# Performance work log

Hardware: AMD Instinct MI355X
Metric: run time of the kernel (lower is better)

Reference implementation:

```python
import jax, jax.numpy as jnp
import numpy as np

HEADS = 8
DIM_HEAD = 128
ATTN_MATRIX_SCALE = 1.5  # tau applied to mean-centered logits
SCALE = DIM_HEAD ** -0.5


def setup_inputs() -> dict:
    key = jax.random.key(0)
    ks = jax.random.split(key, 7)
    b, n, m = 2, 2048, 2048
    qd, cd, inner = 1024, 768, HEADS * DIM_HEAD
    x = jax.random.normal(ks[0], (b, n, qd), dtype=jnp.float32)
    context = jax.random.normal(ks[1], (b, m, cd), dtype=jnp.float32)
    Wq = jax.random.normal(ks[2], (qd, inner), dtype=jnp.float32) * (qd ** -0.5)
    Wk = jax.random.normal(ks[3], (cd, inner), dtype=jnp.float32) * (cd ** -0.5)
    Wv = jax.random.normal(ks[4], (cd, inner), dtype=jnp.float32) * (cd ** -0.5)
    Wout = jax.random.normal(ks[5], (inner, qd), dtype=jnp.float32) * (inner ** -0.5)
    bout = jnp.zeros((qd,), dtype=jnp.float32)
    return {"x": x, "context": context, "Wq": Wq, "Wk": Wk, "Wv": Wv,
            "Wout": Wout, "bout": bout}


def _split_heads(t):
    # (b, n, h*d) -> (h, b*n, d); matches rearrange '(b h) n d -> h (b n) d'
    b, n, _ = t.shape
    t = t.reshape(b, n, HEADS, DIM_HEAD)
    return t.transpose(2, 0, 1, 3).reshape(HEADS, b * n, DIM_HEAD)


def reference(x, context, Wq, Wk, Wv, Wout, bout):
    b, n, _ = x.shape
    qh = _split_heads(jnp.einsum('bnq,qi->bni', x, Wq))        # (h, b*n, d)
    kh = _split_heads(jnp.einsum('bmc,ci->bmi', context, Wk))  # (h, b*m, d)
    vh = _split_heads(jnp.einsum('bmc,ci->bmi', context, Wv))  # (h, b*m, d)

    # custom mean-centered / tau-scaled similarity (_compute_sim_with_tau)
    sim = jnp.einsum('hid,hjd->hij', qh, kh) * SCALE
    mean = jnp.mean(sim, axis=-1, keepdims=True)
    sim = (sim - mean) * ATTN_MATRIX_SCALE + mean

    attn = jax.nn.softmax(sim, axis=-1)
    out = jnp.einsum('hij,hjd->hid', attn, vh)                 # (h, b*n, d)

    # (h, b*n, d) -> (b, n, h*d)
    out = out.reshape(HEADS, b, n, DIM_HEAD).transpose(1, 2, 0, 3)
    out = out.reshape(b, n, HEADS * DIM_HEAD)
    return jnp.einsum('bni,iq->bnq', out, Wout) + bout
```

## Files before the change

### kernel.cpp

```cpp
#include <hip/hip_runtime.h>
#include <cstdint>
#include <cstddef>

typedef unsigned short u16t;
typedef __bf16 bf16x8_t __attribute__((ext_vector_type(8)));
typedef float f32x4_t __attribute__((ext_vector_type(4)));
typedef float f32x16_t __attribute__((ext_vector_type(16)));

#define MFMA_BF16 __builtin_amdgcn_mfma_f32_16x16x32_bf16
#define MFMA32    __builtin_amdgcn_mfma_f32_32x32x16_bf16

__device__ __forceinline__ u16t f2bf(float f) {
    uint32_t u = __builtin_bit_cast(uint32_t, f);
    u += 0x7fffu + ((u >> 16) & 1u);
    return (u16t)(u >> 16);
}

__device__ __forceinline__ uint32_t pk2bf(float a, float b) {
    return (uint32_t)f2bf(a) | ((uint32_t)f2bf(b) << 16);
}

__device__ __forceinline__ float bflo(uint32_t u) {
    return __builtin_bit_cast(float, u << 16);
}
__device__ __forceinline__ float bfhi(uint32_t u) {
    return __builtin_bit_cast(float, u & 0xffff0000u);
}

__device__ __forceinline__ bf16x8_t ld_frag(const u16t* p) {
    return __builtin_bit_cast(bf16x8_t, *(const uint4*)p);
}

__device__ __forceinline__ uint32_t cvtpk(float lo, float hi) {
    uint32_t r;
    asm("v_cvt_pk_bf16_f32 %0, %1, %2" : "=v"(r) : "v"(lo), "v"(hi));
    return r;
}
__device__ __forceinline__ void swap32(uint32_t& a, uint32_t& b) {
    asm("v_permlane32_swap_b32 %0, %1" : "+v"(a), "+v"(b));
}

__device__ __forceinline__ void gl_lds16(const u16t* g, u16t* l) {
    __builtin_amdgcn_global_load_lds(
        (const __attribute__((address_space(1))) void*)g,
        (__attribute__((address_space(3))) void*)l, 16, 0, 0);
}

__global__ void cast2_bf16_kernel(const float* __restrict__ s0, u16t* __restrict__ d0, int n0,
                                  const float* __restrict__ s1, u16t* __restrict__ d1, int n1) {
    int i = blockIdx.x * blockDim.x + threadIdx.x;
    const float* s; u16t* d;
    if (i < n0) { s = s0; d = d0; }
    else { i -= n0; if (i >= n1) return; s = s1; d = d1; }
    float4 v = ((const float4*)s)[i];
    uint2 o;
    o.x = pk2bf(v.x, v.y);
    o.y = pk2bf(v.z, v.w);
    ((uint2*)d)[i] = o;
}

__global__ void transpose4_kernel(const float* __restrict__ Wq, const float* __restrict__ Wk,
                                  const float* __restrict__ Wv, const float* __restrict__ Wo,
                                  u16t* __restrict__ Wqt, u16t* __restrict__ Wkt,
                                  u16t* __restrict__ Wvt, u16t* __restrict__ Wot) {
    const int z = blockIdx.z;
    const float* W = z == 0 ? Wq : (z == 1 ? Wk : (z == 2 ? Wv : Wo));
    u16t* Wt      = z == 0 ? Wqt : (z == 1 ? Wkt : (z == 2 ? Wvt : Wot));
    const int K   = (z == 1 || z == 2) ? 768 : 1024;
    const int N = 1024;
    int n0 = blockIdx.x * 32, k0 = blockIdx.y * 32;
    if (k0 >= K) return;
    __shared__ float tile[32][33];
    int tx = threadIdx.x, ty = threadIdx.y;
    for (int i = ty; i < 32; i += 8)
        tile[i][tx] = W[(size_t)(k0 + i) * N + n0 + tx];
    __syncthreads();
    for (int i = ty; i < 32; i += 8)
        Wt[(size_t)(n0 + i) * K + k0 + tx] = f2bf(tile[tx][i]);
}

__device__ __forceinline__ void gemm_core(
    const u16t* __restrict__ A, const u16t* __restrict__ Bt,
    int K, void* __restrict__ outp, const float* __restrict__ bias,
    int mode, float oscale, int bm, int bn)
{
    __shared__ __align__(16) u16t As[2][128 * 64];
    __shared__ __align__(16) u16t Bs[2][64 * 64];
    const int tid = threadIdx.x;
    const int wave = tid >> 6, lane = tid & 63;
    const int wm = wave & 1, wn = wave >> 1;
    const int quad = lane >> 4, l16 = lane & 15;

    const int l8r = lane >> 3, l8c = lane & 7;
    const int cgx = (l8c ^ l8r) * 8;

    f32x4_t acc[4][2];
#pragma unroll
    for (int i = 0; i < 4; ++i)
#pragma unroll
        for (int j = 0; j < 2; ++j) acc[i][j] = (f32x4_t){0.f, 0.f, 0.f, 0.f};

    const int nk = K >> 6;

#pragma unroll
    for (int it = 0; it < 4; ++it) {
        int rb = wave * 32 + it * 8;
        gl_lds16(&A[(size_t)(bm + rb + l8r) * K + cgx], &As[0][rb * 64]);
    }
#pragma unroll
    for (int it = 0; it < 2; ++it) {
        int rb = wave * 16 + it * 8;
        gl_lds16(&Bt[(size_t)(bn + rb + l8r) * K + cgx], &Bs[0][rb * 64]);
    }

    for (int ki = 0; ki < nk; ++ki) {
        const int buf = ki & 1;
        __syncthreads();

        if (ki + 1 < nk) {
            const int kc = (ki + 1) << 6;
#pragma unroll
            for (int it = 0; it < 4; ++it) {
                int rb = wave * 32 + it * 8;
                gl_lds16(&A[(size_t)(bm + rb + l8r) * K + kc + cgx], &As[buf ^ 1][rb * 64]);
            }
#pragma unroll
            for (int it = 0; it < 2; ++it) {
                int rb = wave * 16 + it * 8;
                gl_lds16(&Bt[(size_t)(bn + rb + l8r) * K + kc + cgx], &Bs[buf ^ 1][rb * 64]);
            }
        }

#pragma unroll
        for (int ks = 0; ks < 2; ++ks) {
            bf16x8_t af[4], bfv[2];
#pragma unroll
            for (int i = 0; i < 4; ++i) {
                int r = wm * 64 + i * 16 + l16;
                af[i] = ld_frag(&As[buf][r * 64 + (((ks * 4 + quad) ^ (r & 7)) * 8)]);
            }
#pragma unroll
            for (int j = 0; j < 2; ++j) {
                int r = wn * 32 + j * 16 + l16;
                bfv[j] = ld_frag(&Bs[buf][r * 64 + (((ks * 4 + quad) ^ (r & 7)) * 8)]);
            }
#pragma unroll
            for (int i = 0; i < 4; ++i)
#pragma unroll
                for (int j = 0; j < 2; ++j)
                    acc[i][j] = MFMA_BF16(af[i], bfv[j], acc[i][j], 0, 0, 0);
        }
    }

    if (mode == 3) {
        float* out = (float*)outp;
#pragma unroll
        for (int j = 0; j < 2; ++j) {
            int c = bn + wn * 32 + j * 16 + l16;
            float b = bias[c];
#pragma unroll
            for (int i = 0; i < 4; ++i) {
                int rb = bm + wm * 64 + i * 16 + quad * 4;
#pragma unroll
                for (int r = 0; r < 4; ++r)
                    out[(size_t)(rb + r) * 1024 + c] = acc[i][j][r] + b;
            }
        }
    } else if (mode == 2) {
        u16t* out = (u16t*)outp;
#pragma unroll
        for (int i = 0; i < 4; ++i)
#pragma unroll
            for (int j = 0; j < 2; ++j) {
                int rb = bm + wm * 64 + i * 16 + quad * 4;
                int c = bn + wn * 32 + j * 16 + l16;
                int h = c >> 7, d = c & 127;
                uint2 pk;
                pk.x = pk2bf(acc[i][j][0], acc[i][j][1]);
                pk.y = pk2bf(acc[i][j][2], acc[i][j][3]);
                *(uint2*)&out[((size_t)h * 128 + d) * 4096 + rb] = pk;
            }
    } else {
        u16t* out = (u16t*)outp;
#pragma unroll
        for (int i = 0; i < 4; ++i)
#pragma unroll
            for (int j = 0; j < 2; ++j) {
                int rb = bm + wm * 64 + i * 16 + quad * 4;
                int c = bn + wn * 32 + j * 16 + l16;
                int h = c >> 7, d = c & 127;
#pragma unroll
                for (int r = 0; r < 4; ++r)
                    out[((size_t)h * 4096 + rb + r) * 128 + d] = f2bf(acc[i][j][r] * oscale);
            }
    }
}

__global__ __launch_bounds__(256) void gemm_bf16_kernel(
    const u16t* __restrict__ A, const u16t* __restrict__ Bt,
    int K, void* __restrict__ outp, const float* __restrict__ bias,
    int mode, float oscale)
{
    gemm_core(A, Bt, K, outp, bias, mode, oscale, blockIdx.y * 128, blockIdx.x * 64);
}

__global__ __launch_bounds__(256) void qkv_kernel(
    const u16t* __restrict__ x_bf, const u16t* __restrict__ ctx_bf,
    const u16t* __restrict__ Wqt, const u16t* __restrict__ Wkt,
    const u16t* __restrict__ Wvt,
    u16t* __restrict__ Qh, u16t* __restrict__ Kh, u16t* __restrict__ Vt,
    float qscale)
{
    const int z = blockIdx.z;
    const u16t* A  = (z == 0) ? x_bf : ctx_bf;
    const u16t* Bt = (z == 0) ? Wqt : ((z == 1) ? Wkt : Wvt);
    void* outp     = (z == 0) ? (void*)Qh : ((z == 1) ? (void*)Kh : (void*)Vt);
    const int K    = (z == 0) ? 1024 : 768;
    const int mode = (z == 2) ? 2 : 0;
    const float sc = (z == 0) ? qscale : 1.0f;
    gemm_core(A, Bt, K, outp, nullptr, mode, sc, blockIdx.y * 128, blockIdx.x * 64);
}

__global__ __launch_bounds__(256) void flash_kernel(
    const u16t* __restrict__ Qh, const u16t* __restrict__ Kh,
    const u16t* __restrict__ Vtg, u16t* __restrict__ Op0,
    u16t* __restrict__ Op1, float* __restrict__ lp)
{
    extern __shared__ __align__(16) u16t smem[];
    const int h = blockIdx.y;
    const int q0 = blockIdx.x * 128;
    const int z = blockIdx.z;
    const int tid = threadIdx.x;
    const int wave = tid >> 6, lane = tid & 63;
    const int l31 = lane & 31, hh = lane >> 5;

    const u16t* Kg = Kh + (size_t)h * 4096 * 128 + (size_t)z * 2048 * 128;
    const u16t* Vg = Vtg + (size_t)h * 128 * 4096 + z * 2048;

    {
        const u16t* Qg = Qh + ((size_t)h * 4096 + q0) * 128;
#pragma unroll
        for (int it = 0; it < 8; ++it) {
            int slot = it * 256 + tid;
            int r = slot >> 4, c = slot & 15;
            uint4 v = *(const uint4*)&Qg[(size_t)r * 128 + c * 8];
            *(uint4*)&smem[r * 128 + ((c ^ (r & 15)) * 8)] = v;
        }
    }
    __syncthreads();
    bf16x8_t qf[8];
    {
        int r = wave * 32 + l31;
#pragma unroll
        for (int s = 0; s < 8; ++s)
            qf[s] = ld_frag(&smem[r * 128 + (((s * 2 + hh) ^ (r & 15)) * 8)]);
    }
    __syncthreads();

    const bool kRole = wave < 2;
    const int wh = wave & 1;
    const int rK = lane >> 4, cK = lane & 15;
    const int rV = lane >> 2, cV = lane & 3;

    if (kRole) {
#pragma unroll
        for (int it = 0; it < 4; ++it) {
            int is = wh * 4 + it;
            int rowL = is * 4 + rK;
            gl_lds16(Kg + (size_t)rowL * 128 + ((cK ^ (rowL & 15)) * 8),
                     smem + is * 512);
        }
    } else {
#pragma unroll
        for (int it = 0; it < 4; ++it) {
            int is = wh * 4 + it;
            int rowL = is * 16 + rV;
            gl_lds16(Vg + (size_t)rowL * 4096 + ((cV ^ (rowL & 3)) * 8),
                     smem + 8192 + is * 512);
        }
    }

    f32x16_t O[4];
#pragma unroll
    for (int dg = 0; dg < 4; ++dg)
#pragma unroll
        for (int r = 0; r < 16; ++r) O[dg][r] = 0.f;
    float lsum = 0.f;

    for (int kb = 0; kb < 64; ++kb) {
        const int buf = kb & 1;
        __syncthreads();

        if (kb < 63) {
            const int j0 = (kb + 1) * 32;
            const int bo = (buf ^ 1) * 4096;
            if (kRole) {
#pragma unroll
                for (int it = 0; it < 4; ++it) {
                    int is = wh * 4 + it;
                    int rowL = is * 4 + rK;
                    gl_lds16(Kg + (size_t)(j0 + rowL) * 128 + ((cK ^ (rowL & 15)) * 8),
                             smem + bo + is * 512);
                }
            } else {
#pragma unroll
                for (int it = 0; it < 4; ++it) {
                    int is = wh * 4 + it;
                    int rowL = is * 16 + rV;
                    gl_lds16(Vg + (size_t)rowL * 4096 + j0 + ((cV ^ (rowL & 3)) * 8),
                             smem + 8192 + bo + is * 512);
                }
            }
        }

        const u16t* Ks = smem + buf * 4096;
        const u16t* Vs = smem + 8192 + buf * 4096;

        f32x16_t Sa, Sb;
#pragma unroll
        for (int r = 0; r < 16; ++r) { Sa[r] = 0.f; Sb[r] = 0.f; }
        const int swz = l31 & 15;
#pragma unroll
        for (int s = 0; s < 8; s += 2) {
            bf16x8_t k0 = ld_frag(&Ks[l31 * 128 + (((s * 2 + hh) ^ swz) * 8)]);
            bf16x8_t k1 = ld_frag(&Ks[l31 * 128 + ((((s + 1) * 2 + hh) ^ swz) * 8)]);
            Sa = MFMA32(k0, qf[s], Sa, 0, 0, 0);
            Sb = MFMA32(k1, qf[s + 1], Sb, 0, 0, 0);
        }

        float p[16];
#pragma unroll
        for (int r = 0; r < 16; ++r)
            p[r] = __builtin_amdgcn_exp2f(Sa[r] + Sb[r]);
        lsum += ((((p[0] + p[1]) + (p[2] + p[3])) + ((p[4] + p[5]) + (p[6] + p[7])))
              + (((p[8] + p[9]) + (p[10] + p[11])) + ((p[12] + p[13]) + (p[14] + p[15]))));

        uint32_t w0 = cvtpk(p[0], p[1]),   w2 = cvtpk(p[4], p[5]);
        uint32_t w1 = cvtpk(p[2], p[3]),   w3 = cvtpk(p[6], p[7]);
        swap32(w0, w2); swap32(w1, w3);
        uint32_t y0 = cvtpk(p[8], p[9]),   y2 = cvtpk(p[12], p[13]);
        uint32_t y1 = cvtpk(p[10], p[11]), y3 = cvtpk(p[14], p[15]);
        swap32(y0, y2); swap32(y1, y3);
        uint4 pw0; pw0.x = w0; pw0.y = w1; pw0.z = w2; pw0.w = w3;
        uint4 pw1; pw1.x = y0; pw1.y = y1; pw1.z = y2; pw1.w = y3;
        bf16x8_t pf0 = __builtin_bit_cast(bf16x8_t, pw0);
        bf16x8_t pf1 = __builtin_bit_cast(bf16x8_t, pw1);

#pragma unroll
        for (int dg = 0; dg < 4; ++dg) {
            int rv = dg * 32 + l31;
            int vsw = rv & 3;
            bf16x8_t v0 = ld_frag(&Vs[rv * 32 + ((hh ^ vsw) * 8)]);
            bf16x8_t v1 = ld_frag(&Vs[rv * 32 + (((2 + hh) ^ vsw) * 8)]);
            O[dg] = MFMA32(v0, pf0, O[dg], 0, 0, 0);
            O[dg] = MFMA32(v1, pf1, O[dg], 0, 0, 0);
        }
    }

    lsum += __shfl_xor(lsum, 32, 64);
    u16t* Op = z ? Op1 : Op0;
    const int qrow = q0 + wave * 32 + l31;
    if (lane < 32) lp[z * 32768 + qrow * 8 + h] = lsum;
#pragma unroll
    for (int dg = 0; dg < 4; ++dg)
#pragma unroll
        for (int rq = 0; rq < 4; ++rq) {
            uint2 pk;
            pk.x = pk2bf(O[dg][rq * 4 + 0], O[dg][rq * 4 + 1]);
            pk.y = pk2bf(O[dg][rq * 4 + 2], O[dg][rq * 4 + 3]);
            *(uint2*)&Op[(size_t)qrow * 1024 + h * 128 + dg * 32 + rq * 8 + hh * 4] = pk;
        }
}

__global__ __launch_bounds__(256) void combine_kernel(
    const u16t* __restrict__ O0, const u16t* __restrict__ O1,
    const float* __restrict__ lp, u16t* __restrict__ out)
{
    int t = blockIdx.x * blockDim.x + threadIdx.x;
    int e = t << 3;
    int i = e >> 10, h = (e >> 7) & 7;
    float inv = 1.f / (lp[i * 8 + h] + lp[32768 + i * 8 + h]);
    uint4 a = ((const uint4*)O0)[t];
    uint4 b = ((const uint4*)O1)[t];
    uint4 r;
    r.x = pk2bf((bflo(a.x) + bflo(b.x)) * inv, (bfhi(a.x) + bfhi(b.x)) * inv);
    r.y = pk2bf((bflo(a.y) + bflo(b.y)) * inv, (bfhi(a.y) + bfhi(b.y)) * inv);
    r.z = pk2bf((bflo(a.z) + bflo(b.z)) * inv, (bfhi(a.z) + bfhi(b.z)) * inv);
    r.w = pk2bf((bflo(a.w) + bflo(b.w)) * inv, (bfhi(a.w) + bfhi(b.w)) * inv);
    ((uint4*)out)[t] = r;
}

extern "C" void kernel_launch(void* const* d_in, const int* in_sizes, int n_in,
                              void* d_out, int out_size, void* d_ws, size_t ws_size,
                              hipStream_t stream)
{
    (void)in_sizes; (void)n_in; (void)out_size; (void)ws_size;
    const float* x    = (const float*)d_in[0];
    const float* ctx  = (const float*)d_in[1];
    const float* Wq   = (const float*)d_in[2];
    const float* Wk   = (const float*)d_in[3];
    const float* Wv   = (const float*)d_in[4];
    const float* Wout = (const float*)d_in[5];
    const float* bout = (const float*)d_in[6];
    float* out = (float*)d_out;

    u16t* ws = (u16t*)d_ws;
    u16t* x_bf   = ws;
    u16t* ctx_bf = x_bf + 4194304;
    u16t* Wqt    = ctx_bf + 3145728;
    u16t* Wkt    = Wqt + 1048576;
    u16t* Wvt    = Wkt + 786432;
    u16t* Woutt  = Wvt + 786432;
    u16t* Qh     = Woutt + 1048576;
    u16t* Kh     = Qh + 4194304;
    u16t* Vt     = Kh + 4194304;
    u16t* Oh   = x_bf;
    u16t* Ohp1 = ws + 4194304;
    float* lp  = (float*)(ws + 8388608);

    constexpr float QSCALE = 1.5f * 0.08838834764831845f * 1.4426950408889634f;

    (void)hipFuncSetAttribute((const void*)flash_kernel,
                              hipFuncAttributeMaxDynamicSharedMemorySize, 32768);

    cast2_bf16_kernel<<<7168, 256, 0, stream>>>(x, x_bf, 1048576, ctx, ctx_bf, 786432);
    transpose4_kernel<<<dim3(32, 32, 4), dim3(32, 8), 0, stream>>>(
        Wq, Wk, Wv, Wout, Wqt, Wkt, Wvt, Woutt);

    qkv_kernel<<<dim3(16, 32, 3), 256, 0, stream>>>(
        x_bf, ctx_bf, Wqt, Wkt, Wvt, Qh, Kh, Vt, QSCALE);

    flash_kernel<<<dim3(32, 8, 2), 256, 32768, stream>>>(Qh, Kh, Vt, Oh, Ohp1, lp);
    combine_kernel<<<2048, 256, 0, stream>>>(Oh, Ohp1, lp, Oh);

    gemm_bf16_kernel<<<dim3(16, 32), 256, 0, stream>>>(Oh, Woutt, 1024, out, bout, 3, 1.0f);
}
```

Before: 254.2 us.

## Process two 32-row query groups per wave in flash attention to reuse K/V fragments

Each wave of the flash kernel now owns 64 query rows, in two 32-row groups, instead of 32. Every K and V fragment loaded from LDS feeds twice as many MFMAs, and the number of blocks that stream K/V through shared memory is halved. The grid shrinks to 256 blocks with 64KB of dynamic shared memory for Q staging, and launch bounds allow one block per CU. The cost is a large rise in register use for the doubled accumulators and Q fragments, and only four waves per CU to hide latency.

```diff
diff --git a/kernel.cpp b/kernel.cpp
--- a/kernel.cpp
+++ b/kernel.cpp
@@ -221,14 +221,14 @@
     gemm_core(A, Bt, K, outp, nullptr, mode, sc, blockIdx.y * 128, blockIdx.x * 64);
 }
 
-__global__ __launch_bounds__(256) void flash_kernel(
+__global__ __launch_bounds__(256, 1) void flash_kernel(
     const u16t* __restrict__ Qh, const u16t* __restrict__ Kh,
     const u16t* __restrict__ Vtg, u16t* __restrict__ Op0,
     u16t* __restrict__ Op1, float* __restrict__ lp)
 {
     extern __shared__ __align__(16) u16t smem[];
     const int h = blockIdx.y;
-    const int q0 = blockIdx.x * 128;
+    const int q0 = blockIdx.x * 256;
     const int z = blockIdx.z;
     const int tid = threadIdx.x;
     const int wave = tid >> 6, lane = tid & 63;
@@ -240,7 +240,7 @@
     {
         const u16t* Qg = Qh + ((size_t)h * 4096 + q0) * 128;
 #pragma unroll
-        for (int it = 0; it < 8; ++it) {
+        for (int it = 0; it < 16; ++it) {
             int slot = it * 256 + tid;
             int r = slot >> 4, c = slot & 15;
             uint4 v = *(const uint4*)&Qg[(size_t)r * 128 + c * 8];
@@ -248,12 +248,13 @@
         }
     }
     __syncthreads();
-    bf16x8_t qf[8];
-    {
-        int r = wave * 32 + l31;
+    bf16x8_t qf[2][8];
+#pragma unroll
+    for (int g = 0; g < 2; ++g) {
+        int r = wave * 64 + g * 32 + l31;
 #pragma unroll
         for (int s = 0; s < 8; ++s)
-            qf[s] = ld_frag(&smem[r * 128 + (((s * 2 + hh) ^ (r & 15)) * 8)]);
+            qf[g][s] = ld_frag(&smem[r * 128 + (((s * 2 + hh) ^ (r & 15)) * 8)]);
     }
     __syncthreads();
 
@@ -280,12 +281,15 @@
         }
     }
 
-    f32x16_t O[4];
-#pragma unroll
-    for (int dg = 0; dg < 4; ++dg)
-#pragma unroll
-        for (int r = 0; r < 16; ++r) O[dg][r] = 0.f;
-    float lsum = 0.f;
+    f32x16_t O[2][4];
+#pragma unroll
+    for (int g = 0; g < 2; ++g)
+#pragma unroll
+        for (int dg = 0; dg < 4; ++dg)
+#pragma unroll
+            for (int r = 0; r < 16; ++r) O[g][dg][r] = 0.f;
+    float lsum0 = 0.f, lsum1 = 0.f;
+    const int swz = l31 & 15;
 
     for (int kb = 0; kb < 64; ++kb) {
         const int buf = kb & 1;
@@ -316,35 +320,56 @@
         const u16t* Ks = smem + buf * 4096;
         const u16t* Vs = smem + 8192 + buf * 4096;
 
-        f32x16_t Sa, Sb;
-#pragma unroll
-        for (int r = 0; r < 16; ++r) { Sa[r] = 0.f; Sb[r] = 0.f; }
-        const int swz = l31 & 15;
+        f32x16_t S0a, S0b, S1a, S1b;
+#pragma unroll
+        for (int r = 0; r < 16; ++r) { S0a[r] = 0.f; S0b[r] = 0.f; S1a[r] = 0.f; S1b[r] = 0.f; }
 #pragma unroll
         for (int s = 0; s < 8; s += 2) {
             bf16x8_t k0 = ld_frag(&Ks[l31 * 128 + (((s * 2 + hh) ^ swz) * 8)]);
             bf16x8_t k1 = ld_frag(&Ks[l31 * 128 + ((((s + 1) * 2 + hh) ^ swz) * 8)]);
-            Sa = MFMA32(k0, qf[s], Sa, 0, 0, 0);
-            Sb = MFMA32(k1, qf[s + 1], Sb, 0, 0, 0);
-        }
-
-        float p[16];
-#pragma unroll
-        for (int r = 0; r < 16; ++r)
-            p[r] = __builtin_amdgcn_exp2f(Sa[r] + Sb[r]);
-        lsum += ((((p[0] + p[1]) + (p[2] + p[3])) + ((p[4] + p[5]) + (p[6] + p[7])))
-              + (((p[8] + p[9]) + (p[10] + p[11])) + ((p[12] + p[13]) + (p[14] + p[15]))));
-
-        uint32_t w0 = cvtpk(p[0], p[1]),   w2 = cvtpk(p[4], p[5]);
-        uint32_t w1 = cvtpk(p[2], p[3]),   w3 = cvtpk(p[6], p[7]);
-        swap32(w0, w2); swap32(w1, w3);
-        uint32_t y0 = cvtpk(p[8], p[9]),   y2 = cvtpk(p[12], p[13]);
-        uint32_t y1 = cvtpk(p[10], p[11]), y3 = cvtpk(p[14], p[15]);
-        swap32(y0, y2); swap32(y1, y3);
-        uint4 pw0; pw0.x = w0; pw0.y = w1; pw0.z = w2; pw0.w = w3;
-        uint4 pw1; pw1.x = y0; pw1.y = y1; pw1.z = y2; pw1.w = y3;
-        bf16x8_t pf0 = __builtin_bit_cast(bf16x8_t, pw0);
-        bf16x8_t pf1 = __builtin_bit_cast(bf16x8_t, pw1);
+            S0a = MFMA32(k0, qf[0][s], S0a, 0, 0, 0);
+            S1a = MFMA32(k0, qf[1][s], S1a, 0, 0, 0);
+            S0b = MFMA32(k1, qf[0][s + 1], S0b, 0, 0, 0);
+            S1b = MFMA32(k1, qf[1][s + 1], S1b, 0, 0, 0);
+        }
+
+        bf16x8_t pf[2][2];
+        {
+            float p[16];
+#pragma unroll
+            for (int r = 0; r < 16; ++r)
+                p[r] = __builtin_amdgcn_exp2f(S0a[r] + S0b[r]);
+            lsum0 += ((((p[0] + p[1]) + (p[2] + p[3])) + ((p[4] + p[5]) + (p[6] + p[7])))
+                   + (((p[8] + p[9]) + (p[10] + p[11])) + ((p[12] + p[13]) + (p[14] + p[15]))));
+            uint32_t w0 = cvtpk(p[0], p[1]),   w2 = cvtpk(p[4], p[5]);
+            uint32_t w1 = cvtpk(p[2], p[3]),   w3 = cvtpk(p[6], p[7]);
+            swap32(w0, w2); swap32(w1, w3);
+            uint32_t y0 = cvtpk(p[8], p[9]),   y2 = cvtpk(p[12], p[13]);
+            uint32_t y1 = cvtpk(p[10], p[11]), y3 = cvtpk(p[14], p[15]);
+            swap32(y0, y2); swap32(y1, y3);
+            uint4 pw0; pw0.x = w0; pw0.y = w1; pw0.z = w2; pw0.w = w3;
+            uint4 pw1; pw1.x = y0; pw1.y = y1; pw1.z = y2; pw1.w = y3;
+            pf[0][0] = __builtin_bit_cast(bf16x8_t, pw0);
+            pf[0][1] = __builtin_bit_cast(bf16x8_t, pw1);
+        }
+        {
+            float p[16];
+#pragma unroll
+            for (int r = 0; r < 16; ++r)
+                p[r] = __builtin_amdgcn_exp2f(S1a[r] + S1b[r]);
+            lsum1 += ((((p[0] + p[1]) + (p[2] + p[3])) + ((p[4] + p[5]) + (p[6] + p[7])))
+                   + (((p[8] + p[9]) + (p[10] + p[11])) + ((p[12] + p[13]) + (p[14] + p[15]))));
+            uint32_t w0 = cvtpk(p[0], p[1]),   w2 = cvtpk(p[4], p[5]);
+            uint32_t w1 = cvtpk(p[2], p[3]),   w3 = cvtpk(p[6], p[7]);
+            swap32(w0, w2); swap32(w1, w3);
+            uint32_t y0 = cvtpk(p[8], p[9]),   y2 = cvtpk(p[12], p[13]);
+            uint32_t y1 = cvtpk(p[10], p[11]), y3 = cvtpk(p[14], p[15]);
+            swap32(y0, y2); swap32(y1, y3);
+            uint4 pw0; pw0.x = w0; pw0.y = w1; pw0.z = w2; pw0.w = w3;
+            uint4 pw1; pw1.x = y0; pw1.y = y1; pw1.z = y2; pw1.w = y3;
+            pf[1][0] = __builtin_bit_cast(bf16x8_t, pw0);
+            pf[1][1] = __builtin_bit_cast(bf16x8_t, pw1);
+        }
 
 #pragma unroll
         for (int dg = 0; dg < 4; ++dg) {
@@ -352,24 +377,30 @@
             int vsw = rv & 3;
             bf16x8_t v0 = ld_frag(&Vs[rv * 32 + ((hh ^ vsw) * 8)]);
             bf16x8_t v1 = ld_frag(&Vs[rv * 32 + (((2 + hh) ^ vsw) * 8)]);
-            O[dg] = MFMA32(v0, pf0, O[dg], 0, 0, 0);
-            O[dg] = MFMA32(v1, pf1, O[dg], 0, 0, 0);
-        }
-    }
-
-    lsum += __shfl_xor(lsum, 32, 64);
+            O[0][dg] = MFMA32(v0, pf[0][0], O[0][dg], 0, 0, 0);
+            O[0][dg] = MFMA32(v1, pf[0][1], O[0][dg], 0, 0, 0);
+            O[1][dg] = MFMA32(v0, pf[1][0], O[1][dg], 0, 0, 0);
+            O[1][dg] = MFMA32(v1, pf[1][1], O[1][dg], 0, 0, 0);
+        }
+    }
+
     u16t* Op = z ? Op1 : Op0;
-    const int qrow = q0 + wave * 32 + l31;
-    if (lane < 32) lp[z * 32768 + qrow * 8 + h] = lsum;
-#pragma unroll
-    for (int dg = 0; dg < 4; ++dg)
-#pragma unroll
-        for (int rq = 0; rq < 4; ++rq) {
-            uint2 pk;
-            pk.x = pk2bf(O[dg][rq * 4 + 0], O[dg][rq * 4 + 1]);
-            pk.y = pk2bf(O[dg][rq * 4 + 2], O[dg][rq * 4 + 3]);
-            *(uint2*)&Op[(size_t)qrow * 1024 + h * 128 + dg * 32 + rq * 8 + hh * 4] = pk;
-        }
+#pragma unroll
+    for (int g = 0; g < 2; ++g) {
+        float ls = g ? lsum1 : lsum0;
+        ls += __shfl_xor(ls, 32, 64);
+        const int qrow = q0 + wave * 64 + g * 32 + l31;
+        if (lane < 32) lp[z * 32768 + qrow * 8 + h] = ls;
+#pragma unroll
+        for (int dg = 0; dg < 4; ++dg)
+#pragma unroll
+            for (int rq = 0; rq < 4; ++rq) {
+                uint2 pk;
+                pk.x = pk2bf(O[g][dg][rq * 4 + 0], O[g][dg][rq * 4 + 1]);
+                pk.y = pk2bf(O[g][dg][rq * 4 + 2], O[g][dg][rq * 4 + 3]);
+                *(uint2*)&Op[(size_t)qrow * 1024 + h * 128 + dg * 32 + rq * 8 + hh * 4] = pk;
+            }
+    }
 }
 
 __global__ __launch_bounds__(256) void combine_kernel(
@@ -421,7 +452,7 @@
     constexpr float QSCALE = 1.5f * 0.08838834764831845f * 1.4426950408889634f;
 
     (void)hipFuncSetAttribute((const void*)flash_kernel,
-                              hipFuncAttributeMaxDynamicSharedMemorySize, 32768);
+                              hipFuncAttributeMaxDynamicSharedMemorySize, 65536);
 
     cast2_bf16_kernel<<<7168, 256, 0, stream>>>(x, x_bf, 1048576, ctx, ctx_bf, 786432);
     transpose4_kernel<<<dim3(32, 32, 4), dim3(32, 8), 0, stream>>>(
@@ -430,7 +461,7 @@
     qkv_kernel<<<dim3(16, 32, 3), 256, 0, stream>>>(
         x_bf, ctx_bf, Wqt, Wkt, Wvt, Qh, Kh, Vt, QSCALE);
 
-    flash_kernel<<<dim3(32, 8, 2), 256, 32768, stream>>>(Qh, Kh, Vt, Oh, Ohp1, lp);
+    flash_kernel<<<dim3(16, 8, 2), 256, 65536, stream>>>(Qh, Kh, Vt, Oh, Ohp1, lp);
     combine_kernel<<<2048, 256, 0, stream>>>(Oh, Ohp1, lp, Oh);
 
     gemm_bf16_kernel<<<dim3(16, 32), 256, 0, stream>>>(Oh, Woutt, 1024, out, bout, 3, 1.0f);
```

After: 255.3 us. About the same (+0.5%).

## Warp-specialize flash kernel into QK/softmax and PV producer-consumer waves

Applied to the files above, without the earlier changes.

Splits the flash attention block into two wave roles. Two waves compute QK^T and the exponentials for 64 query rows each and write bf16 P tiles to a double-buffered LDS region. The other two waves consume those tiles one step later, multiplying by V for a 64-column slice of the head dimension. The aim is to overlap the softmax/exp work with the PV MFMAs and stop recomputing fragments per wave. It costs an extra LDS round trip for P and more shared memory (53 KB), and adds launch bounds targeting 2 blocks per CU; each role also has idle MFMA phases.

```diff
diff --git a/kernel.cpp b/kernel.cpp
--- a/kernel.cpp
+++ b/kernel.cpp
@@ -221,7 +221,7 @@
     gemm_core(A, Bt, K, outp, nullptr, mode, sc, blockIdx.y * 128, blockIdx.x * 64);
 }
 
-__global__ __launch_bounds__(256) void flash_kernel(
+__global__ __launch_bounds__(256, 2) void flash_kernel(
     const u16t* __restrict__ Qh, const u16t* __restrict__ Kh,
     const u16t* __restrict__ Vtg, u16t* __restrict__ Op0,
     u16t* __restrict__ Op1, float* __restrict__ lp)
@@ -233,39 +233,28 @@
     const int tid = threadIdx.x;
     const int wave = tid >> 6, lane = tid & 63;
     const int l31 = lane & 31, hh = lane >> 5;
+    const int NT = 64;
 
     const u16t* Kg = Kh + (size_t)h * 4096 * 128 + (size_t)z * 2048 * 128;
     const u16t* Vg = Vtg + (size_t)h * 128 * 4096 + z * 2048;
 
-    {
-        const u16t* Qg = Qh + ((size_t)h * 4096 + q0) * 128;
-#pragma unroll
-        for (int it = 0; it < 8; ++it) {
-            int slot = it * 256 + tid;
-            int r = slot >> 4, c = slot & 15;
-            uint4 v = *(const uint4*)&Qg[(size_t)r * 128 + c * 8];
-            *(uint4*)&smem[r * 128 + ((c ^ (r & 15)) * 8)] = v;
-        }
-    }
-    __syncthreads();
-    bf16x8_t qf[8];
-    {
-        int r = wave * 32 + l31;
-#pragma unroll
-        for (int s = 0; s < 8; ++s)
-            qf[s] = ld_frag(&smem[r * 128 + (((s * 2 + hh) ^ (r & 15)) * 8)]);
-    }
-    __syncthreads();
-
-    const bool kRole = wave < 2;
-    const int wh = wave & 1;
+    const bool sRole = wave < 2;
     const int rK = lane >> 4, cK = lane & 15;
     const int rV = lane >> 2, cV = lane & 3;
 
-    if (kRole) {
+    bf16x8_t qf[2][8];
+    if (sRole) {
+        const u16t* Qg = Qh + ((size_t)h * 4096 + q0) * 128;
+#pragma unroll
+        for (int c = 0; c < 2; ++c) {
+            int qr = wave * 64 + c * 32 + l31;
+#pragma unroll
+            for (int s = 0; s < 8; ++s)
+                qf[c][s] = ld_frag(&Qg[(size_t)qr * 128 + s * 16 + hh * 8]);
+        }
 #pragma unroll
         for (int it = 0; it < 4; ++it) {
-            int is = wh * 4 + it;
+            int is = wave * 4 + it;
             int rowL = is * 4 + rK;
             gl_lds16(Kg + (size_t)rowL * 128 + ((cK ^ (rowL & 15)) * 8),
                      smem + is * 512);
@@ -273,103 +262,137 @@
     } else {
 #pragma unroll
         for (int it = 0; it < 4; ++it) {
-            int is = wh * 4 + it;
+            int is = (wave - 2) * 4 + it;
             int rowL = is * 16 + rV;
             gl_lds16(Vg + (size_t)rowL * 4096 + ((cV ^ (rowL & 3)) * 8),
                      smem + 8192 + is * 512);
         }
     }
 
-    f32x16_t O[4];
-#pragma unroll
-    for (int dg = 0; dg < 4; ++dg)
-#pragma unroll
-        for (int r = 0; r < 16; ++r) O[dg][r] = 0.f;
-    float lsum = 0.f;
-
-    for (int kb = 0; kb < 64; ++kb) {
-        const int buf = kb & 1;
+    f32x16_t O[2][4];
+#pragma unroll
+    for (int dg = 0; dg < 2; ++dg)
+#pragma unroll
+        for (int qc = 0; qc < 4; ++qc)
+#pragma unroll
+            for (int r = 0; r < 16; ++r) O[dg][qc][r] = 0.f;
+    float lsum[2] = {0.f, 0.f};
+
+    for (int t = 0; t <= NT; ++t) {
         __syncthreads();
 
-        if (kb < 63) {
-            const int j0 = (kb + 1) * 32;
-            const int bo = (buf ^ 1) * 4096;
-            if (kRole) {
-#pragma unroll
-                for (int it = 0; it < 4; ++it) {
-                    int is = wh * 4 + it;
-                    int rowL = is * 4 + rK;
-                    gl_lds16(Kg + (size_t)(j0 + rowL) * 128 + ((cK ^ (rowL & 15)) * 8),
-                             smem + bo + is * 512);
-                }
-            } else {
-#pragma unroll
-                for (int it = 0; it < 4; ++it) {
-                    int is = wh * 4 + it;
-                    int rowL = is * 16 + rV;
-                    gl_lds16(Vg + (size_t)rowL * 4096 + j0 + ((cV ^ (rowL & 3)) * 8),
-                             smem + 8192 + bo + is * 512);
-                }
-            }
-        }
-
-        const u16t* Ks = smem + buf * 4096;
-        const u16t* Vs = smem + 8192 + buf * 4096;
-
-        f32x16_t Sa, Sb;
-#pragma unroll
-        for (int r = 0; r < 16; ++r) { Sa[r] = 0.f; Sb[r] = 0.f; }
-        const int swz = l31 & 15;
-#pragma unroll
-        for (int s = 0; s < 8; s += 2) {
-            bf16x8_t k0 = ld_frag(&Ks[l31 * 128 + (((s * 2 + hh) ^ swz) * 8)]);
-            bf16x8_t k1 = ld_frag(&Ks[l31 * 128 + ((((s + 1) * 2 + hh) ^ swz) * 8)]);
-            Sa = MFMA32(k0, qf[s], Sa, 0, 0, 0);
-            Sb = MFMA32(k1, qf[s + 1], Sb, 0, 0, 0);
-        }
-
-        float p[16];
-#pragma unroll
-        for (int r = 0; r < 16; ++r)
-            p[r] = __builtin_amdgcn_exp2f(Sa[r] + Sb[r]);
-        lsum += ((((p[0] + p[1]) + (p[2] + p[3])) + ((p[4] + p[5]) + (p[6] + p[7])))
-              + (((p[8] + p[9]) + (p[10] + p[11])) + ((p[12] + p[13]) + (p[14] + p[15]))));
-
-        uint32_t w0 = cvtpk(p[0], p[1]),   w2 = cvtpk(p[4], p[5]);
-        uint32_t w1 = cvtpk(p[2], p[3]),   w3 = cvtpk(p[6], p[7]);
-        swap32(w0, w2); swap32(w1, w3);
-        uint32_t y0 = cvtpk(p[8], p[9]),   y2 = cvtpk(p[12], p[13]);
-        uint32_t y1 = cvtpk(p[10], p[11]), y3 = cvtpk(p[14], p[15]);
-        swap32(y0, y2); swap32(y1, y3);
-        uint4 pw0; pw0.x = w0; pw0.y = w1; pw0.z = w2; pw0.w = w3;
-        uint4 pw1; pw1.x = y0; pw1.y = y1; pw1.z = y2; pw1.w = y3;
-        bf16x8_t pf0 = __builtin_bit_cast(bf16x8_t, pw0);
-        bf16x8_t pf1 = __builtin_bit_cast(bf16x8_t, pw1);
-
-#pragma unroll
-        for (int dg = 0; dg < 4; ++dg) {
-            int rv = dg * 32 + l31;
-            int vsw = rv & 3;
-            bf16x8_t v0 = ld_frag(&Vs[rv * 32 + ((hh ^ vsw) * 8)]);
-            bf16x8_t v1 = ld_frag(&Vs[rv * 32 + (((2 + hh) ^ vsw) * 8)]);
-            O[dg] = MFMA32(v0, pf0, O[dg], 0, 0, 0);
-            O[dg] = MFMA32(v1, pf1, O[dg], 0, 0, 0);
-        }
-    }
-
-    lsum += __shfl_xor(lsum, 32, 64);
+        if (sRole) {
+            if (t < NT) {
+                if (t + 1 < NT) {
+                    const int j0 = (t + 1) * 32;
+                    u16t* kd = smem + ((t + 1) & 1) * 4096;
+#pragma unroll
+                    for (int it = 0; it < 4; ++it) {
+                        int is = wave * 4 + it;
+                        int rowL = is * 4 + rK;
+                        gl_lds16(Kg + (size_t)(j0 + rowL) * 128 + ((cK ^ (rowL & 15)) * 8),
+                                 kd + is * 512);
+                    }
+                }
+                const u16t* kb = smem + (t & 1) * 4096;
+                u16t* pw = smem + 16384 + (t & 1) * 5120;
+
+                f32x16_t S0, S1;
+#pragma unroll
+                for (int r = 0; r < 16; ++r) { S0[r] = 0.f; S1[r] = 0.f; }
+#pragma unroll
+                for (int s = 0; s < 8; ++s) {
+                    bf16x8_t kf = ld_frag(&kb[l31 * 128 + (((s * 2 + hh) ^ (l31 & 15)) * 8)]);
+                    S0 = MFMA32(kf, qf[0][s], S0, 0, 0, 0);
+                    S1 = MFMA32(kf, qf[1][s], S1, 0, 0, 0);
+                }
+
+#pragma unroll
+                for (int c = 0; c < 2; ++c) {
+                    float p[16];
+#pragma unroll
+                    for (int r = 0; r < 16; ++r)
+                        p[r] = __builtin_amdgcn_exp2f(c ? S1[r] : S0[r]);
+                    lsum[c] += ((((p[0] + p[1]) + (p[2] + p[3])) + ((p[4] + p[5]) + (p[6] + p[7])))
+                             + (((p[8] + p[9]) + (p[10] + p[11])) + ((p[12] + p[13]) + (p[14] + p[15]))));
+                    uint32_t w0 = cvtpk(p[0], p[1]),   w2 = cvtpk(p[4], p[5]);
+                    uint32_t w1 = cvtpk(p[2], p[3]),   w3 = cvtpk(p[6], p[7]);
+                    swap32(w0, w2); swap32(w1, w3);
+                    uint32_t y0 = cvtpk(p[8], p[9]),   y2 = cvtpk(p[12], p[13]);
+                    uint32_t y1 = cvtpk(p[10], p[11]), y3 = cvtpk(p[14], p[15]);
+                    swap32(y0, y2); swap32(y1, y3);
+                    uint4 pw0; pw0.x = w0; pw0.y = w1; pw0.z = w2; pw0.w = w3;
+                    uint4 pw1; pw1.x = y0; pw1.y = y1; pw1.z = y2; pw1.w = y3;
+                    int qloc = wave * 64 + c * 32 + l31;
+                    *(uint4*)&pw[qloc * 40 + hh * 8] = pw0;
+                    *(uint4*)&pw[qloc * 40 + 16 + hh * 8] = pw1;
+                }
+            }
+        } else {
+            if (t >= 1) {
+                if (t < NT) {
+                    const int j0 = t * 32;
+                    u16t* vd = smem + 8192 + (t & 1) * 4096;
+#pragma unroll
+                    for (int it = 0; it < 4; ++it) {
+                        int is = (wave - 2) * 4 + it;
+                        int rowL = is * 16 + rV;
+                        gl_lds16(Vg + (size_t)rowL * 4096 + j0 + ((cV ^ (rowL & 3)) * 8),
+                                 vd + is * 512);
+                    }
+                }
+                const u16t* vb = smem + 8192 + ((t - 1) & 1) * 4096;
+                const u16t* pb = smem + 16384 + ((t - 1) & 1) * 5120;
+
+                bf16x8_t pf[4][2];
+#pragma unroll
+                for (int qc = 0; qc < 4; ++qc)
+#pragma unroll
+                    for (int ks = 0; ks < 2; ++ks)
+                        pf[qc][ks] = ld_frag(&pb[(qc * 32 + l31) * 40 + ks * 16 + hh * 8]);
+#pragma unroll
+                for (int dg = 0; dg < 2; ++dg) {
+                    int rv = (wave - 2) * 64 + dg * 32 + l31;
+                    int vsw = rv & 3;
+                    bf16x8_t v0 = ld_frag(&vb[rv * 32 + ((hh ^ vsw) * 8)]);
+                    bf16x8_t v1 = ld_frag(&vb[rv * 32 + (((2 + hh) ^ vsw) * 8)]);
+#pragma unroll
+                    for (int qc = 0; qc < 4; ++qc) {
+                        O[dg][qc] = MFMA32(v0, pf[qc][0], O[dg][qc], 0, 0, 0);
+                        O[dg][qc] = MFMA32(v1, pf[qc][1], O[dg][qc], 0, 0, 0);
+                    }
+                }
+            }
+        }
+    }
+
     u16t* Op = z ? Op1 : Op0;
-    const int qrow = q0 + wave * 32 + l31;
-    if (lane < 32) lp[z * 32768 + qrow * 8 + h] = lsum;
-#pragma unroll
-    for (int dg = 0; dg < 4; ++dg)
-#pragma unroll
-        for (int rq = 0; rq < 4; ++rq) {
-            uint2 pk;
-            pk.x = pk2bf(O[dg][rq * 4 + 0], O[dg][rq * 4 + 1]);
-            pk.y = pk2bf(O[dg][rq * 4 + 2], O[dg][rq * 4 + 3]);
-            *(uint2*)&Op[(size_t)qrow * 1024 + h * 128 + dg * 32 + rq * 8 + hh * 4] = pk;
-        }
+    if (sRole) {
+#pragma unroll
+        for (int c = 0; c < 2; ++c) {
+            float ls = lsum[c];
+            ls += __shfl_xor(ls, 32, 64);
+            if (hh == 0) {
+                int qrow = q0 + wave * 64 + c * 32 + l31;
+                lp[z * 32768 + qrow * 8 + h] = ls;
+            }
+        }
+    } else {
+        const int wvoff = (wave - 2) * 64;
+#pragma unroll
+        for (int qc = 0; qc < 4; ++qc) {
+            size_t base = (size_t)(q0 + qc * 32 + l31) * 1024 + h * 128;
+#pragma unroll
+            for (int dg = 0; dg < 2; ++dg)
+#pragma unroll
+                for (int g = 0; g < 4; ++g) {
+                    uint2 pk;
+                    pk.x = pk2bf(O[dg][qc][g * 4 + 0], O[dg][qc][g * 4 + 1]);
+                    pk.y = pk2bf(O[dg][qc][g * 4 + 2], O[dg][qc][g * 4 + 3]);
+                    *(uint2*)&Op[base + wvoff + dg * 32 + g * 8 + hh * 4] = pk;
+                }
+        }
+    }
 }
 
 __global__ __launch_bounds__(256) void combine_kernel(
@@ -421,7 +444,7 @@
     constexpr float QSCALE = 1.5f * 0.08838834764831845f * 1.4426950408889634f;
 
     (void)hipFuncSetAttribute((const void*)flash_kernel,
-                              hipFuncAttributeMaxDynamicSharedMemorySize, 32768);
+                              hipFuncAttributeMaxDynamicSharedMemorySize, 53248);
 
     cast2_bf16_kernel<<<7168, 256, 0, stream>>>(x, x_bf, 1048576, ctx, ctx_bf, 786432);
     transpose4_kernel<<<dim3(32, 32, 4), dim3(32, 8), 0, stream>>>(
@@ -430,7 +453,7 @@
     qkv_kernel<<<dim3(16, 32, 3), 256, 0, stream>>>(
         x_bf, ctx_bf, Wqt, Wkt, Wvt, Qh, Kh, Vt, QSCALE);
 
-    flash_kernel<<<dim3(32, 8, 2), 256, 32768, stream>>>(Qh, Kh, Vt, Oh, Ohp1, lp);
+    flash_kernel<<<dim3(32, 8, 2), 256, 53248, stream>>>(Qh, Kh, Vt, Oh, Ohp1, lp);
     combine_kernel<<<2048, 256, 0, stream>>>(Oh, Ohp1, lp, Oh);
 
     gemm_bf16_kernel<<<dim3(16, 32), 256, 0, stream>>>(Oh, Woutt, 1024, out, bout, 3, 1.0f);
```

Result: slower. 316.1 us (+24.4%).

## Software-pipeline flash loop: overlap PV of previous tile with QK of current

Applied to the files above, without the earlier changes.

Restructures the flash attention main loop so each iteration runs the P·V MFMAs for the previous key tile while computing QKᵀ, exp2 and bf16 packing for the current tile. V tiles move to a triple-buffered LDS ring, raising dynamic LDS to 40 KB, so the in-flight prefetch does not overwrite the tile still being read. It also adds a min-blocks-per-CU hint of 2 to launch bounds. The intent is to hide the exp/convert latency behind matrix work. The cost is higher register pressure from keeping P fragments live across iterations, plus a dead unused accumulator array.

```diff
diff --git a/kernel.cpp b/kernel.cpp
--- a/kernel.cpp
+++ b/kernel.cpp
@@ -221,7 +221,7 @@
     gemm_core(A, Bt, K, outp, nullptr, mode, sc, blockIdx.y * 128, blockIdx.x * 64);
 }
 
-__global__ __launch_bounds__(256) void flash_kernel(
+__global__ __launch_bounds__(256, 2) void flash_kernel(
     const u16t* __restrict__ Qh, const u16t* __restrict__ Kh,
     const u16t* __restrict__ Vtg, u16t* __restrict__ Op0,
     u16t* __restrict__ Op1, float* __restrict__ lp)
@@ -233,6 +233,7 @@
     const int tid = threadIdx.x;
     const int wave = tid >> 6, lane = tid & 63;
     const int l31 = lane & 31, hh = lane >> 5;
+    const int NT = 64;
 
     const u16t* Kg = Kh + (size_t)h * 4096 * 128 + (size_t)z * 2048 * 128;
     const u16t* Vg = Vtg + (size_t)h * 128 * 4096 + z * 2048;
@@ -280,95 +281,116 @@
         }
     }
 
-    f32x16_t O[4];
+    f32x4_t O[8];
+#pragma unroll
+    for (int dt = 0; dt < 8; ++dt) O[dt] = (f32x4_t){0.f, 0.f, 0.f, 0.f};
+    f32x16_t Ow[4];
 #pragma unroll
     for (int dg = 0; dg < 4; ++dg)
 #pragma unroll
-        for (int r = 0; r < 16; ++r) O[dg][r] = 0.f;
+        for (int r = 0; r < 16; ++r) Ow[dg][r] = 0.f;
+
     float lsum = 0.f;
-
-    for (int kb = 0; kb < 64; ++kb) {
-        const int buf = kb & 1;
+    const int swz = l31 & 15;
+    bf16x8_t pf0, pf1;
+    int v_rd = 2;
+    int v_wr = 1;
+
+    for (int t = 0; t <= NT; ++t) {
         __syncthreads();
 
-        if (kb < 63) {
-            const int j0 = (kb + 1) * 32;
-            const int bo = (buf ^ 1) * 4096;
+        if (t + 1 < NT) {
+            const int j0 = (t + 1) * 32;
             if (kRole) {
+                u16t* kd = smem + ((t + 1) & 1) * 4096;
 #pragma unroll
                 for (int it = 0; it < 4; ++it) {
                     int is = wh * 4 + it;
                     int rowL = is * 4 + rK;
                     gl_lds16(Kg + (size_t)(j0 + rowL) * 128 + ((cK ^ (rowL & 15)) * 8),
-                             smem + bo + is * 512);
+                             kd + is * 512);
                 }
             } else {
+                u16t* vd = smem + 8192 + v_wr * 4096;
 #pragma unroll
                 for (int it = 0; it < 4; ++it) {
                     int is = wh * 4 + it;
                     int rowL = is * 16 + rV;
                     gl_lds16(Vg + (size_t)rowL * 4096 + j0 + ((cV ^ (rowL & 3)) * 8),
-                             smem + 8192 + bo + is * 512);
+                             vd + is * 512);
                 }
             }
         }
 
-        const u16t* Ks = smem + buf * 4096;
-        const u16t* Vs = smem + 8192 + buf * 4096;
-
-        f32x16_t Sa, Sb;
-#pragma unroll
-        for (int r = 0; r < 16; ++r) { Sa[r] = 0.f; Sb[r] = 0.f; }
-        const int swz = l31 & 15;
-#pragma unroll
-        for (int s = 0; s < 8; s += 2) {
-            bf16x8_t k0 = ld_frag(&Ks[l31 * 128 + (((s * 2 + hh) ^ swz) * 8)]);
-            bf16x8_t k1 = ld_frag(&Ks[l31 * 128 + ((((s + 1) * 2 + hh) ^ swz) * 8)]);
-            Sa = MFMA32(k0, qf[s], Sa, 0, 0, 0);
-            Sb = MFMA32(k1, qf[s + 1], Sb, 0, 0, 0);
-        }
-
-        float p[16];
-#pragma unroll
-        for (int r = 0; r < 16; ++r)
-            p[r] = __builtin_amdgcn_exp2f(Sa[r] + Sb[r]);
-        lsum += ((((p[0] + p[1]) + (p[2] + p[3])) + ((p[4] + p[5]) + (p[6] + p[7])))
-              + (((p[8] + p[9]) + (p[10] + p[11])) + ((p[12] + p[13]) + (p[14] + p[15]))));
-
-        uint32_t w0 = cvtpk(p[0], p[1]),   w2 = cvtpk(p[4], p[5]);
-        uint32_t w1 = cvtpk(p[2], p[3]),   w3 = cvtpk(p[6], p[7]);
-        swap32(w0, w2); swap32(w1, w3);
-        uint32_t y0 = cvtpk(p[8], p[9]),   y2 = cvtpk(p[12], p[13]);
-        uint32_t y1 = cvtpk(p[10], p[11]), y3 = cvtpk(p[14], p[15]);
-        swap32(y0, y2); swap32(y1, y3);
-        uint4 pw0; pw0.x = w0; pw0.y = w1; pw0.z = w2; pw0.w = w3;
-        uint4 pw1; pw1.x = y0; pw1.y = y1; pw1.z = y2; pw1.w = y3;
-        bf16x8_t pf0 = __builtin_bit_cast(bf16x8_t, pw0);
-        bf16x8_t pf1 = __builtin_bit_cast(bf16x8_t, pw1);
-
-#pragma unroll
-        for (int dg = 0; dg < 4; ++dg) {
-            int rv = dg * 32 + l31;
-            int vsw = rv & 3;
-            bf16x8_t v0 = ld_frag(&Vs[rv * 32 + ((hh ^ vsw) * 8)]);
-            bf16x8_t v1 = ld_frag(&Vs[rv * 32 + (((2 + hh) ^ vsw) * 8)]);
-            O[dg] = MFMA32(v0, pf0, O[dg], 0, 0, 0);
-            O[dg] = MFMA32(v1, pf1, O[dg], 0, 0, 0);
-        }
-    }
+        if (t >= 1) {
+            const u16t* vb = smem + 8192 + v_rd * 4096;
+#pragma unroll
+            for (int dg = 0; dg < 4; ++dg) {
+                int rv = dg * 32 + l31;
+                int vsw = rv & 3;
+                bf16x8_t v0 = ld_frag(&vb[rv * 32 + ((hh ^ vsw) * 8)]);
+                bf16x8_t v1 = ld_frag(&vb[rv * 32 + (((2 + hh) ^ vsw) * 8)]);
+                Ow[dg] = MFMA32(v0, pf0, Ow[dg], 0, 0, 0);
+                Ow[dg] = MFMA32(v1, pf1, Ow[dg], 0, 0, 0);
+            }
+        }
+
+        if (t < NT) {
+            const u16t* kb = smem + (t & 1) * 4096;
+            f32x16_t Sa, Sb;
+#pragma unroll
+            for (int r = 0; r < 16; ++r) { Sa[r] = 0.f; Sb[r] = 0.f; }
+#pragma unroll
+            for (int s = 0; s < 8; s += 2) {
+                bf16x8_t k0 = ld_frag(&kb[l31 * 128 + (((s * 2 + hh) ^ swz) * 8)]);
+                bf16x8_t k1 = ld_frag(&kb[l31 * 128 + ((((s + 1) * 2 + hh) ^ swz) * 8)]);
+                Sa = MFMA32(k0, qf[s], Sa, 0, 0, 0);
+                Sb = MFMA32(k1, qf[s + 1], Sb, 0, 0, 0);
+            }
+
+            float p[16];
+#pragma unroll
+            for (int r = 0; r < 16; ++r)
+                p[r] = __builtin_amdgcn_exp2f(Sa[r] + Sb[r]);
+            lsum += ((((p[0] + p[1]) + (p[2] + p[3])) + ((p[4] + p[5]) + (p[6] + p[7])))
+                  + (((p[8] + p[9]) + (p[10] + p[11])) + ((p[12] + p[13]) + (p[14] + p[15]))));
+
+            uint32_t w0 = cvtpk(p[0], p[1]),   w2 = cvtpk(p[4], p[5]);
+            uint32_t w1 = cvtpk(p[2], p[3]),   w3 = cvtpk(p[6], p[7]);
+            swap32(w0, w2); swap32(w1, w3);
+            uint32_t y0 = cvtpk(p[8], p[9]),   y2 = cvtpk(p[12], p[13]);
+            uint32_t y1 = cvtpk(p[10], p[11]), y3 = cvtpk(p[14], p[15]);
+            swap32(y0, y2); swap32(y1, y3);
+            uint4 pw0; pw0.x = w0; pw0.y = w1; pw0.z = w2; pw0.w = w3;
+            uint4 pw1; pw1.x = y0; pw1.y = y1; pw1.z = y2; pw1.w = y3;
+            pf0 = __builtin_bit_cast(bf16x8_t, pw0);
+            pf1 = __builtin_bit_cast(bf16x8_t, pw1);
+        }
+
+        v_rd = v_rd + 1 == 3 ? 0 : v_rd + 1;
+        v_wr = v_wr + 1 == 3 ? 0 : v_wr + 1;
+    }
+
+#pragma unroll
+    for (int dg = 0; dg < 4; ++dg)
+#pragma unroll
+        for (int half = 0; half < 2; ++half)
+#pragma unroll
+            for (int r = 0; r < 4; ++r)
+                O[dg * 2 + half][r] = Ow[dg][half * 4 + r] + O[dg * 2 + half][r];
 
     lsum += __shfl_xor(lsum, 32, 64);
     u16t* Op = z ? Op1 : Op0;
-    const int qrow = q0 + wave * 32 + l31;
-    if (lane < 32) lp[z * 32768 + qrow * 8 + h] = lsum;
+    size_t i = (size_t)(q0 + wave * 32 + l31);
+    if (hh == 0) lp[z * 32768 + i * 8 + h] = lsum;
 #pragma unroll
     for (int dg = 0; dg < 4; ++dg)
 #pragma unroll
-        for (int rq = 0; rq < 4; ++rq) {
+        for (int g = 0; g < 4; ++g) {
             uint2 pk;
-            pk.x = pk2bf(O[dg][rq * 4 + 0], O[dg][rq * 4 + 1]);
-            pk.y = pk2bf(O[dg][rq * 4 + 2], O[dg][rq * 4 + 3]);
-            *(uint2*)&Op[(size_t)qrow * 1024 + h * 128 + dg * 32 + rq * 8 + hh * 4] = pk;
+            pk.x = pk2bf(Ow[dg][g * 4 + 0], Ow[dg][g * 4 + 1]);
+            pk.y = pk2bf(Ow[dg][g * 4 + 2], Ow[dg][g * 4 + 3]);
+            *(uint2*)&Op[i * 1024 + h * 128 + dg * 32 + g * 8 + hh * 4] = pk;
         }
 }
 
@@ -421,7 +443,7 @@
     constexpr float QSCALE = 1.5f * 0.08838834764831845f * 1.4426950408889634f;
 
     (void)hipFuncSetAttribute((const void*)flash_kernel,
-                              hipFuncAttributeMaxDynamicSharedMemorySize, 32768);
+                              hipFuncAttributeMaxDynamicSharedMemorySize, 40960);
 
     cast2_bf16_kernel<<<7168, 256, 0, stream>>>(x, x_bf, 1048576, ctx, ctx_bf, 786432);
     transpose4_kernel<<<dim3(32, 32, 4), dim3(32, 8), 0, stream>>>(
@@ -430,7 +452,7 @@
     qkv_kernel<<<dim3(16, 32, 3), 256, 0, stream>>>(
         x_bf, ctx_bf, Wqt, Wkt, Wvt, Qh, Kh, Vt, QSCALE);
 
-    flash_kernel<<<dim3(32, 8, 2), 256, 32768, stream>>>(Qh, Kh, Vt, Oh, Ohp1, lp);
+    flash_kernel<<<dim3(32, 8, 2), 256, 40960, stream>>>(Qh, Kh, Vt, Oh, Ohp1, lp);
     combine_kernel<<<2048, 256, 0, stream>>>(Oh, Ohp1, lp, Oh);
 
     gemm_bf16_kernel<<<dim3(16, 32), 256, 0, stream>>>(Oh, Woutt, 1024, out, bout, 3, 1.0f);
```

Measured after the change: 237.2 us. 6.7% less time.
